# Kernel optimization log

Measured on AMD Instinct MI355X. Metric: run time of the kernel, lower is better.

## Reference

```python
import jax, jax.numpy as jnp
import numpy as np

N = 100_000   # nodes
E = 1_280_000 # edges
F_IN = 64
HID = 64

def setup_inputs() -> dict:
    key = jax.random.key(0)
    ks = jax.random.split(key, 5)
    x = jax.random.normal(ks[0], (N, F_IN), dtype=jnp.float32)
    edge_index = jax.random.randint(ks[1], (2, E), 0, N, dtype=jnp.int32)
    edge_weight = jax.random.uniform(ks[2], (E,), dtype=jnp.float32)
    s1 = 1.0 / np.sqrt(F_IN)
    W1 = jax.random.uniform(ks[3], (F_IN, HID), minval=-s1, maxval=s1, dtype=jnp.float32)
    b1 = jnp.zeros((HID,), jnp.float32)
    s2 = 1.0 / np.sqrt(HID)
    W2 = jax.random.uniform(ks[4], (HID, 1), minval=-s2, maxval=s2, dtype=jnp.float32)
    b2 = jnp.zeros((1,), jnp.float32)
    return {"x": x, "edge_index": edge_index, "edge_weight": edge_weight,
            "W1": W1, "b1": b1, "W2": W2, "b2": b2}


def reference(x, edge_index, edge_weight, W1, b1, W2, b2):
    # eval mode: edge dropout and feature dropout are identity.
    # GCNConv with add_self_loops=True: A_hat = A + I, D_hat^-1/2 A_hat D_hat^-1/2.
    row, col = edge_index[0], edge_index[1]
    sl = jnp.arange(N, dtype=row.dtype)
    row = jnp.concatenate([row, sl])
    col = jnp.concatenate([col, sl])
    w = jnp.concatenate([edge_weight, jnp.ones((N,), edge_weight.dtype)])
    # symmetric normalization (shared by both conv layers)
    deg = jax.ops.segment_sum(w, col, num_segments=N)          # [N]
    dinv = jnp.where(deg > 0, jax.lax.rsqrt(deg), 0.0)
    norm = dinv[row] * w * dinv[col]                           # [E+N]

    def gcn(h):  # h: [N, d] already linearly transformed
        msg = h[row] * norm[:, None]                           # gather + scale
        return jax.ops.segment_sum(msg, col, num_segments=N)   # scatter-add

    h = gcn(x @ W1) + b1          # conv1
    h = jax.nn.relu(h)            # relu (dropout = identity in eval)
    out = gcn(h @ W2) + b2        # conv2 -> [N, 1]
    return out
```

## Files before the change

### kernel.cpp

```cpp
#include <hip/hip_runtime.h>
#include <hip/hip_fp16.h>

#define CNT_SHIFT 26
#define DEG_MASK  ((1u << CNT_SHIFT) - 1)
#define DEG_SCALE 1048576.0f
#define SLAB_LOG 7
#define SLAB 128
#define CAP 2048
#define GSTRIDE 16

typedef __attribute__((ext_vector_type(8))) short short8;
typedef __attribute__((ext_vector_type(4))) float v4f;

__device__ __forceinline__ unsigned short f_to_h16(float f) {
    return __half_as_ushort(__float2half(f));
}
__device__ __forceinline__ float h16_to_f(unsigned short u) {
    return __half2float(__ushort_as_half(u));
}
__device__ __forceinline__ unsigned short f_to_bf16(float f) {
    unsigned int u = __float_as_uint(f);
    u += 0x7fffu + ((u >> 16) & 1u);
    return (unsigned short)(u >> 16);
}
__device__ __forceinline__ unsigned long long mkrec(int r, int c, float wv) {
    return (unsigned long long)r | ((unsigned long long)(c & (SLAB - 1)) << 17)
         | ((unsigned long long)f_to_h16(wv) << 24);
}

__global__ __launch_bounds__(256) void k_scatter_gemm(
        const int4* __restrict__ row4, const int4* __restrict__ col4, const float4* __restrict__ w4,
        const int* __restrict__ row, const int* __restrict__ col, const float* __restrict__ w,
        unsigned* __restrict__ gcur, unsigned long long* __restrict__ binrec,
        const float* __restrict__ x, const float* __restrict__ W1,
        char* __restrict__ h1q, float* __restrict__ scales,
        int E4, int rem, int nBlkE, int nGemm, int n, int nbkt) {
    __shared__ int h[1024];
    int blk = blockIdx.x, t = threadIdx.x;
    if (blk < nBlkE) {
        for (int idx = t; idx < nbkt; idx += 256) h[idx] = 0;
        __syncthreads();
        int base = blk * 1024;
        int4 cs[4];
#pragma unroll
        for (int k = 0; k < 4; ++k) {
            int g = base + k * 256 + t;
            if (g < E4) {
                int4 c = col4[g];
                cs[k] = c;
                atomicAdd(&h[c.x >> SLAB_LOG], 1);
                atomicAdd(&h[c.y >> SLAB_LOG], 1);
                atomicAdd(&h[c.z >> SLAB_LOG], 1);
                atomicAdd(&h[c.w >> SLAB_LOG], 1);
            }
        }
        if (blk == 0 && t < rem) atomicAdd(&h[col[4 * E4 + t] >> SLAB_LOG], 1);
        __syncthreads();
        for (int idx = t; idx < nbkt; idx += 256) {
            int bb = idx + blk;
            while (bb >= nbkt) bb -= nbkt;
            int cnt = h[bb];
            int runbase = 0;
            if (cnt > 0) runbase = (int)atomicAdd(&gcur[(size_t)bb * GSTRIDE], (unsigned)cnt);
            h[bb] = bb * CAP + runbase;
        }
        __syncthreads();
#pragma unroll
        for (int k = 0; k < 4; ++k) {
            int g = base + k * 256 + t;
            if (g < E4) {
                int4   r = row4[g];
                int4   c = cs[k];
                float4 v = w4[g];
                { int pos = atomicAdd(&h[c.x >> SLAB_LOG], 1); binrec[pos] = mkrec(r.x, c.x, v.x); }
                { int pos = atomicAdd(&h[c.y >> SLAB_LOG], 1); binrec[pos] = mkrec(r.y, c.y, v.y); }
                { int pos = atomicAdd(&h[c.z >> SLAB_LOG], 1); binrec[pos] = mkrec(r.z, c.z, v.z); }
                { int pos = atomicAdd(&h[c.w >> SLAB_LOG], 1); binrec[pos] = mkrec(r.w, c.w, v.w); }
            }
        }
        if (blk == 0 && t < rem) {
            int e = 4 * E4 + t;
            int c = col[e];
            int pos = atomicAdd(&h[c >> SLAB_LOG], 1);
            binrec[pos] = mkrec(row[e], c, w[e]);
        }
    } else {
        int b = blk - nBlkE;
        int lane = t & 63;
        int wave = t >> 6;
        int q   = lane >> 4;
        int n16 = lane & 15;
        short8 bf[8];
#pragma unroll
        for (int ct = 0; ct < 4; ++ct) {
#pragma unroll
            for (int hh = 0; hh < 2; ++hh) {
                short8 v;
#pragma unroll
                for (int j = 0; j < 8; ++j)
                    v[j] = (short)f_to_bf16(W1[(hh * 32 + q * 8 + j) * 64 + ct * 16 + n16]);
                bf[ct * 2 + hh] = v;
            }
        }
        int ntile = (n + 15) >> 4;
        int stride = nGemm * 4;
        for (int tile = b * 4 + wave; tile < ntile; tile += stride) {
            int base = tile << 4;
            short8 a0, a1;
            if (base + 16 <= n) {
                const float* xr = x + (size_t)(base + n16) * 64 + q * 8;
                float4 u0 = *(const float4*)(xr);
                float4 u1 = *(const float4*)(xr + 4);
                float4 u2 = *(const float4*)(xr + 32);
                float4 u3 = *(const float4*)(xr + 36);
                a0[0] = (short)f_to_bf16(u0.x); a0[1] = (short)f_to_bf16(u0.y);
                a0[2] = (short)f_to_bf16(u0.z); a0[3] = (short)f_to_bf16(u0.w);
                a0[4] = (short)f_to_bf16(u1.x); a0[5] = (short)f_to_bf16(u1.y);
                a0[6] = (short)f_to_bf16(u1.z); a0[7] = (short)f_to_bf16(u1.w);
                a1[0] = (short)f_to_bf16(u2.x); a1[1] = (short)f_to_bf16(u2.y);
                a1[2] = (short)f_to_bf16(u2.z); a1[3] = (short)f_to_bf16(u2.w);
                a1[4] = (short)f_to_bf16(u3.x); a1[5] = (short)f_to_bf16(u3.y);
                a1[6] = (short)f_to_bf16(u3.z); a1[7] = (short)f_to_bf16(u3.w);
            } else {
                bool ok = (base + n16) < n;
                const float* xr = x + (size_t)(ok ? (base + n16) : 0) * 64 + q * 8;
#pragma unroll
                for (int j = 0; j < 8; ++j) {
                    a0[j] = ok ? (short)f_to_bf16(xr[j])      : (short)0;
                    a1[j] = ok ? (short)f_to_bf16(xr[32 + j]) : (short)0;
                }
            }
            v4f acc0 = {0.f, 0.f, 0.f, 0.f}, acc1 = acc0, acc2 = acc0, acc3 = acc0;
            acc0 = __builtin_amdgcn_mfma_f32_16x16x32_bf16(a0, bf[0], acc0, 0, 0, 0);
            acc0 = __builtin_amdgcn_mfma_f32_16x16x32_bf16(a1, bf[1], acc0, 0, 0, 0);
            acc1 = __builtin_amdgcn_mfma_f32_16x16x32_bf16(a0, bf[2], acc1, 0, 0, 0);
            acc1 = __builtin_amdgcn_mfma_f32_16x16x32_bf16(a1, bf[3], acc1, 0, 0, 0);
            acc2 = __builtin_amdgcn_mfma_f32_16x16x32_bf16(a0, bf[4], acc2, 0, 0, 0);
            acc2 = __builtin_amdgcn_mfma_f32_16x16x32_bf16(a1, bf[5], acc2, 0, 0, 0);
            acc3 = __builtin_amdgcn_mfma_f32_16x16x32_bf16(a0, bf[6], acc3, 0, 0, 0);
            acc3 = __builtin_amdgcn_mfma_f32_16x16x32_bf16(a1, bf[7], acc3, 0, 0, 0);
#pragma unroll
            for (int r = 0; r < 4; ++r) {
                int rowg = base + q * 4 + r;
                if (rowg >= n) break;
                float m = fmaxf(fmaxf(fabsf(acc0[r]), fabsf(acc1[r])),
                                fmaxf(fabsf(acc2[r]), fabsf(acc3[r])));
                m = fmaxf(m, __shfl_xor(m, 1, 64));
                m = fmaxf(m, __shfl_xor(m, 2, 64));
                m = fmaxf(m, __shfl_xor(m, 4, 64));
                m = fmaxf(m, __shfl_xor(m, 8, 64));
                m = fmaxf(m, 1e-20f);
                float inv = 127.0f / m;
                unsigned char* dst = (unsigned char*)h1q + (size_t)rowg * 64 + n16;
                dst[0]  = (unsigned char)(__float2int_rn(acc0[r] * inv) + 128);
                dst[16] = (unsigned char)(__float2int_rn(acc1[r] * inv) + 128);
                dst[32] = (unsigned char)(__float2int_rn(acc2[r] * inv) + 128);
                dst[48] = (unsigned char)(__float2int_rn(acc3[r] * inv) + 128);
                if (n16 == 0) scales[rowg] = m * (1.0f / 127.0f);
            }
        }
    }
}

__global__ __launch_bounds__(256) void k_bucket(
        const unsigned long long* __restrict__ binrec, const unsigned* __restrict__ gcur,
        float* __restrict__ dinv, int* __restrict__ off, int* __restrict__ bktend,
        unsigned* __restrict__ ep, float* __restrict__ scales,
        int N, int nbkt) {
    __shared__ unsigned cnt[SLAB];
    __shared__ int   loff[SLAB];
    __shared__ int   wtot;
    int b = blockIdx.x, t = threadIdx.x;
    int lane = t & 63;
    int e0 = b * CAP;
    int tot = (int)gcur[(size_t)b * GSTRIDE];
    int e1 = e0 + tot;
    if (t < SLAB) cnt[t] = 0u;
    __syncthreads();
    unsigned epw[8];
    unsigned crk[8];
#pragma unroll
    for (int k = 0; k < 8; ++k) {
        int i = e0 + t + k * 256;
        if (i < e1) {
            unsigned long long rec = binrec[i];
            int cl = (int)((rec >> 17) & (SLAB - 1));
            unsigned hb = (unsigned)((rec >> 24) & 0xFFFF);
            float wv = h16_to_f((unsigned short)hb);
            unsigned old = atomicAdd(&cnt[cl],
                                     (1u << CNT_SHIFT) + (unsigned)(wv * DEG_SCALE + 0.5f));
            unsigned rank = old >> CNT_SHIFT;
            epw[k] = ((unsigned)(rec & 0x1FFFF) << 15) | (hb & 0x7fffu);
            crk[k] = ((unsigned)cl << 16) | rank;
        }
    }
    __syncthreads();
    unsigned pk = 0u;
    int c = 0;
    if (t < SLAB) { pk = cnt[t]; c = (int)(pk >> CNT_SHIFT); }
    int incl = c;
#pragma unroll
    for (int o = 1; o < 64; o <<= 1) {
        int v = __shfl_up(incl, o, 64);
        if (lane >= o) incl += v;
    }
    if (t == 63) wtot = incl;
    __syncthreads();
    if (t >= 64 && t < SLAB) incl += wtot;
    if (t < SLAB) {
        int excl = incl - c;
        loff[t] = excl;
        int id = (b << SLAB_LOG) + t;
        if (id < N) {
            float d = rsqrtf((float)(pk & DEG_MASK) * (1.0f / DEG_SCALE) + 1.0f);
            dinv[id] = d;
            scales[id] *= d;
            off[id] = e0 + excl;
        }
    }
    if (t == 0) bktend[b] = e1;
    __syncthreads();
#pragma unroll
    for (int k = 0; k < 8; ++k) {
        int i = e0 + t + k * 256;
        if (i < e1) {
            int cl   = (int)(crk[k] >> 16);
            int rank = (int)(crk[k] & 0xFFFFu);
            ep[e0 + loff[cl] + rank] = epw[k];
        }
    }
}

__global__ __launch_bounds__(256) void k_agg1(
        const char* __restrict__ h1q_, const float* __restrict__ scales,
        const int* __restrict__ off, const int* __restrict__ bktend,
        const unsigned* __restrict__ ep,
        const float* __restrict__ dinv, const float* __restrict__ b1,
        const float* __restrict__ W2,
        float* __restrict__ h2, int n) {
    const unsigned char* __restrict__ h1q = (const unsigned char*)h1q_;
    __shared__ uint2 tbl[4][4][65];
    int t = threadIdx.x;
    int lane = t & 63, wave = t >> 6, grp = lane >> 4, f15 = lane & 15, fl = f15 * 4;
    int i = blockIdx.x * 16 + wave * 4 + grp;
    bool alive = i < n;
    int s = 0, s1 = 0;
    if (alive) {
        s = off[i];
        s1 = (((i & (SLAB - 1)) == (SLAB - 1)) || (i == n - 1)) ? bktend[i >> SLAB_LOG] : off[i + 1];
    }
    int deg = s1 - s;
    int md = max(deg, __shfl_xor(deg, 16, 64));
    md = max(md, __shfl_xor(md, 32, 64));
    float di = alive ? dinv[i] : 0.f;
    float4 acc = {0.f, 0.f, 0.f, 0.f};
    float S = 0.f;
    if (alive) {
        unsigned q4 = *(const unsigned*)(h1q + ((size_t)i << 6) + fl);
        float si = scales[i];
        acc.x = (float)(q4 & 0xffu)         * si;
        acc.y = (float)((q4 >> 8) & 0xffu)  * si;
        acc.z = (float)((q4 >> 16) & 0xffu) * si;
        acc.w = (float)(q4 >> 24)           * si;
        S = si;
    }
    for (int c0 = 0; c0 < md; c0 += 64) {
        int remg = deg - c0;
        int mrem = md - c0; if (mrem > 64) mrem = 64;
        for (int k = 0; k * 16 < mrem; ++k) {
            int slot = k * 16 + f15;
            unsigned src = 0u; float m = 0.f;
            if (slot < remg) {
                unsigned e = ep[s + c0 + slot];
                src = e >> 15;
                m = scales[src] * h16_to_f((unsigned short)(e & 0x7fffu));
            }
            tbl[wave][grp][slot] = make_uint2(src, __float_as_uint(m));
        }
        for (int j = 0; j < mrem; j += 4) {
            uint2 t0 = tbl[wave][grp][j];
            uint2 t1 = tbl[wave][grp][j + 1];
            uint2 t2 = tbl[wave][grp][j + 2];
            uint2 t3 = tbl[wave][grp][j + 3];
            unsigned q0 = *(const unsigned*)(h1q + ((size_t)t0.x << 6) + fl);
            unsigned q1 = *(const unsigned*)(h1q + ((size_t)t1.x << 6) + fl);
            unsigned q2 = *(const unsigned*)(h1q + ((size_t)t2.x << 6) + fl);
            unsigned q3 = *(const unsigned*)(h1q + ((size_t)t3.x << 6) + fl);
            float m0 = __uint_as_float(t0.y), m1 = __uint_as_float(t1.y);
            float m2 = __uint_as_float(t2.y), m3 = __uint_as_float(t3.y);
            acc.x = fmaf((float)(q0 & 0xffu),         m0, acc.x);
            acc.y = fmaf((float)((q0 >> 8) & 0xffu),  m0, acc.y);
            acc.z = fmaf((float)((q0 >> 16) & 0xffu), m0, acc.z);
            acc.w = fmaf((float)(q0 >> 24),           m0, acc.w);
            acc.x = fmaf((float)(q1 & 0xffu),         m1, acc.x);
            acc.y = fmaf((float)((q1 >> 8) & 0xffu),  m1, acc.y);
            acc.z = fmaf((float)((q1 >> 16) & 0xffu), m1, acc.z);
            acc.w = fmaf((float)(q1 >> 24),           m1, acc.w);
            acc.x = fmaf((float)(q2 & 0xffu),         m2, acc.x);
            acc.y = fmaf((float)((q2 >> 8) & 0xffu),  m2, acc.y);
            acc.z = fmaf((float)((q2 >> 16) & 0xffu), m2, acc.z);
            acc.w = fmaf((float)(q2 >> 24),           m2, acc.w);
            acc.x = fmaf((float)(q3 & 0xffu),         m3, acc.x);
            acc.y = fmaf((float)((q3 >> 8) & 0xffu),  m3, acc.y);
            acc.z = fmaf((float)((q3 >> 16) & 0xffu), m3, acc.z);
            acc.w = fmaf((float)(q3 >> 24),           m3, acc.w);
            S += (m0 + m1) + (m2 + m3);
        }
    }
    acc.x = fmaf(S, -128.f, acc.x);
    acc.y = fmaf(S, -128.f, acc.y);
    acc.z = fmaf(S, -128.f, acc.z);
    acc.w = fmaf(S, -128.f, acc.w);
    float4 bb = *(const float4*)(b1 + fl);
    float4 ww = *(const float4*)(W2 + fl);
    float p = fmaxf(fmaf(di, acc.x, bb.x), 0.f) * ww.x
            + fmaxf(fmaf(di, acc.y, bb.y), 0.f) * ww.y
            + fmaxf(fmaf(di, acc.z, bb.z), 0.f) * ww.z
            + fmaxf(fmaf(di, acc.w, bb.w), 0.f) * ww.w;
#pragma unroll
    for (int o = 1; o < 16; o <<= 1) p += __shfl_xor(p, o, 64);
    if (f15 == 0 && alive) h2[i] = di * p;
}

__global__ void k_agg2(const float* __restrict__ h2,
                       const int* __restrict__ off, const int* __restrict__ bktend,
                       const unsigned* __restrict__ ep, const float* __restrict__ dinv,
                       const float* __restrict__ b2, float* __restrict__ out, int n) {
    int i = blockIdx.x * 256 + threadIdx.x;
    if (i >= n) return;
    float acc = h2[i];
    int s = off[i];
    int s1 = (((i & (SLAB - 1)) == (SLAB - 1)) || (i == n - 1)) ? bktend[i >> SLAB_LOG] : off[i + 1];
    for (; s + 8 <= s1; s += 8) {
        unsigned e0 = ep[s],     e1 = ep[s + 1], e2 = ep[s + 2], e3 = ep[s + 3];
        unsigned e4 = ep[s + 4], e5 = ep[s + 5], e6 = ep[s + 6], e7 = ep[s + 7];
        float v0 = h2[e0 >> 15], v1 = h2[e1 >> 15], v2 = h2[e2 >> 15], v3 = h2[e3 >> 15];
        float v4 = h2[e4 >> 15], v5 = h2[e5 >> 15], v6 = h2[e6 >> 15], v7 = h2[e7 >> 15];
        acc = fmaf(v0, h16_to_f((unsigned short)(e0 & 0x7fff)), acc);
        acc = fmaf(v1, h16_to_f((unsigned short)(e1 & 0x7fff)), acc);
        acc = fmaf(v2, h16_to_f((unsigned short)(e2 & 0x7fff)), acc);
        acc = fmaf(v3, h16_to_f((unsigned short)(e3 & 0x7fff)), acc);
        acc = fmaf(v4, h16_to_f((unsigned short)(e4 & 0x7fff)), acc);
        acc = fmaf(v5, h16_to_f((unsigned short)(e5 & 0x7fff)), acc);
        acc = fmaf(v6, h16_to_f((unsigned short)(e6 & 0x7fff)), acc);
        acc = fmaf(v7, h16_to_f((unsigned short)(e7 & 0x7fff)), acc);
    }
    for (; s + 4 <= s1; s += 4) {
        unsigned e0 = ep[s], e1 = ep[s + 1], e2 = ep[s + 2], e3 = ep[s + 3];
        float v0 = h2[e0 >> 15], v1 = h2[e1 >> 15], v2 = h2[e2 >> 15], v3 = h2[e3 >> 15];
        acc = fmaf(v0, h16_to_f((unsigned short)(e0 & 0x7fff)), acc);
        acc = fmaf(v1, h16_to_f((unsigned short)(e1 & 0x7fff)), acc);
        acc = fmaf(v2, h16_to_f((unsigned short)(e2 & 0x7fff)), acc);
        acc = fmaf(v3, h16_to_f((unsigned short)(e3 & 0x7fff)), acc);
    }
    for (; s < s1; ++s) {
        unsigned e = ep[s];
        acc = fmaf(h2[e >> 15], h16_to_f((unsigned short)(e & 0x7fff)), acc);
    }
    out[i] = dinv[i] * acc + b2[0];
}

extern "C" void kernel_launch(void* const* d_in, const int* in_sizes, int n_in,
                              void* d_out, int out_size, void* d_ws, size_t ws_size,
                              hipStream_t stream) {
    const float* x  = (const float*)d_in[0];
    const int*   ei = (const int*)d_in[1];
    const float* w  = (const float*)d_in[2];
    const float* W1 = (const float*)d_in[3];
    const float* b1 = (const float*)d_in[4];
    const float* W2 = (const float*)d_in[5];
    const float* b2 = (const float*)d_in[6];
    float* out = (float*)d_out;

    const int N = in_sizes[0] / 64;
    const int E = in_sizes[2];
    const int* row = ei;
    const int* col = ei + E;

    const int nbkt  = (N + SLAB - 1) >> SLAB_LOG;
    const int E4    = E / 4;
    const int rem   = E - 4 * E4;
    const int nBlkE = (E4 + 1023) / 1024;
    const int nGemm = 1024;

    char* p = (char*)d_ws;
    auto take = [&](size_t bytes) { char* q = p; p += (bytes + 15) & ~(size_t)15; return q; };
    unsigned long long* binrec = (unsigned long long*)take((size_t)nbkt * CAP * 8);
    unsigned* gcur = (unsigned*)take((size_t)nbkt * GSTRIDE * 4);
    int* bktend  = (int*)take((size_t)nbkt * 4);
    char* h1q    = (char*)take((size_t)N * 64);
    float* scales= (float*)take((size_t)N * 4);
    float* dinv  = (float*)take((size_t)N * 4);
    int*   off   = (int*)take((size_t)(N + 1) * 4);
    unsigned* ep = (unsigned*)take((size_t)nbkt * CAP * 4);
    float* h2    = (float*)take((size_t)N * 4);

    (void)hipMemsetAsync(gcur, 0, (size_t)nbkt * GSTRIDE * 4, stream);
    k_scatter_gemm<<<nBlkE + nGemm, 256, 0, stream>>>(
        (const int4*)row, (const int4*)col, (const float4*)w,
        row, col, w, gcur, binrec, x, W1, h1q, scales,
        E4, rem, nBlkE, nGemm, N, nbkt);
    k_bucket<<<nbkt, 256, 0, stream>>>(binrec, gcur, dinv, off, bktend, ep, scales, N, nbkt);
    k_agg1<<<(N + 15) / 16, 256, 0, stream>>>(h1q, scales, off, bktend, ep, dinv, b1, W2, h2, N);
    k_agg2<<<(N + 255) / 256, 256, 0, stream>>>(h2, off, bktend, ep, dinv, b2, out, N);
}
```

Before: 161.9 us.

## Replace two-level bucket sort with global atomic count, scan, and place

Replaces the slab-binned intermediate records and the per-bucket local sort with three steps. Per-node degree and count come from global atomics, a per-slab scan builds offsets and cursors, and a placement pass scatters packed edge words using atomic cursors. This removes the 8-byte binrec staging buffer and its extra read/write pass. In exchange it relies on heavily contended global atomics per edge, reads the edge arrays twice, and adds a kernel launch. Edge order within a node becomes nondeterministic.

Measured after the change: 270.2 us. 1.67x slower.

```diff
diff --git a/kernel.cpp b/kernel.cpp
--- a/kernel.cpp
+++ b/kernel.cpp
@@ -7,7 +7,6 @@
 #define SLAB_LOG 7
 #define SLAB 128
 #define CAP 2048
-#define GSTRIDE 16
 
 typedef __attribute__((ext_vector_type(8))) short short8;
 typedef __attribute__((ext_vector_type(4))) float v4f;
@@ -23,69 +22,41 @@
     u += 0x7fffu + ((u >> 16) & 1u);
     return (unsigned short)(u >> 16);
 }
-__device__ __forceinline__ unsigned long long mkrec(int r, int c, float wv) {
-    return (unsigned long long)r | ((unsigned long long)(c & (SLAB - 1)) << 17)
-         | ((unsigned long long)f_to_h16(wv) << 24);
-}
-
-__global__ __launch_bounds__(256) void k_scatter_gemm(
-        const int4* __restrict__ row4, const int4* __restrict__ col4, const float4* __restrict__ w4,
-        const int* __restrict__ row, const int* __restrict__ col, const float* __restrict__ w,
-        unsigned* __restrict__ gcur, unsigned long long* __restrict__ binrec,
+__device__ __forceinline__ unsigned packcnt(float wv) {
+    return (1u << CNT_SHIFT) + (unsigned)(wv * DEG_SCALE + 0.5f);
+}
+__device__ __forceinline__ unsigned mkep(int r, float wv) {
+    return ((unsigned)r << 15) | (f_to_h16(wv) & 0x7fffu);
+}
+
+__global__ __launch_bounds__(256) void k_count_gemm(
+        const int4* __restrict__ col4, const float4* __restrict__ w4,
+        const int* __restrict__ col, const float* __restrict__ w,
+        unsigned* __restrict__ cnt,
         const float* __restrict__ x, const float* __restrict__ W1,
         char* __restrict__ h1q, float* __restrict__ scales,
-        int E4, int rem, int nBlkE, int nGemm, int n, int nbkt) {
-    __shared__ int h[1024];
+        int E4, int rem, int nCnt, int nGemm, int n) {
     int blk = blockIdx.x, t = threadIdx.x;
-    if (blk < nBlkE) {
-        for (int idx = t; idx < nbkt; idx += 256) h[idx] = 0;
-        __syncthreads();
+    if (blk < nCnt) {
         int base = blk * 1024;
-        int4 cs[4];
 #pragma unroll
         for (int k = 0; k < 4; ++k) {
             int g = base + k * 256 + t;
             if (g < E4) {
-                int4 c = col4[g];
-                cs[k] = c;
-                atomicAdd(&h[c.x >> SLAB_LOG], 1);
-                atomicAdd(&h[c.y >> SLAB_LOG], 1);
-                atomicAdd(&h[c.z >> SLAB_LOG], 1);
-                atomicAdd(&h[c.w >> SLAB_LOG], 1);
-            }
-        }
-        if (blk == 0 && t < rem) atomicAdd(&h[col[4 * E4 + t] >> SLAB_LOG], 1);
-        __syncthreads();
-        for (int idx = t; idx < nbkt; idx += 256) {
-            int bb = idx + blk;
-            while (bb >= nbkt) bb -= nbkt;
-            int cnt = h[bb];
-            int runbase = 0;
-            if (cnt > 0) runbase = (int)atomicAdd(&gcur[(size_t)bb * GSTRIDE], (unsigned)cnt);
-            h[bb] = bb * CAP + runbase;
-        }
-        __syncthreads();
-#pragma unroll
-        for (int k = 0; k < 4; ++k) {
-            int g = base + k * 256 + t;
-            if (g < E4) {
-                int4   r = row4[g];
-                int4   c = cs[k];
+                int4   c = col4[g];
                 float4 v = w4[g];
-                { int pos = atomicAdd(&h[c.x >> SLAB_LOG], 1); binrec[pos] = mkrec(r.x, c.x, v.x); }
-                { int pos = atomicAdd(&h[c.y >> SLAB_LOG], 1); binrec[pos] = mkrec(r.y, c.y, v.y); }
-                { int pos = atomicAdd(&h[c.z >> SLAB_LOG], 1); binrec[pos] = mkrec(r.z, c.z, v.z); }
-                { int pos = atomicAdd(&h[c.w >> SLAB_LOG], 1); binrec[pos] = mkrec(r.w, c.w, v.w); }
+                atomicAdd(&cnt[c.x], packcnt(v.x));
+                atomicAdd(&cnt[c.y], packcnt(v.y));
+                atomicAdd(&cnt[c.z], packcnt(v.z));
+                atomicAdd(&cnt[c.w], packcnt(v.w));
             }
         }
         if (blk == 0 && t < rem) {
             int e = 4 * E4 + t;
-            int c = col[e];
-            int pos = atomicAdd(&h[c >> SLAB_LOG], 1);
-            binrec[pos] = mkrec(row[e], c, w[e]);
+            atomicAdd(&cnt[col[e]], packcnt(w[e]));
         }
     } else {
-        int b = blk - nBlkE;
+        int b = blk - nCnt;
         int lane = t & 63;
         int wave = t >> 6;
         int q   = lane >> 4;
@@ -162,72 +133,59 @@
     }
 }
 
-__global__ __launch_bounds__(256) void k_bucket(
-        const unsigned long long* __restrict__ binrec, const unsigned* __restrict__ gcur,
-        float* __restrict__ dinv, int* __restrict__ off, int* __restrict__ bktend,
-        unsigned* __restrict__ ep, float* __restrict__ scales,
-        int N, int nbkt) {
-    __shared__ unsigned cnt[SLAB];
-    __shared__ int   loff[SLAB];
-    __shared__ int   wtot;
+__global__ __launch_bounds__(128) void k_scan(
+        const unsigned* __restrict__ cnt,
+        float* __restrict__ dinv, int* __restrict__ off, int* __restrict__ cursor,
+        int* __restrict__ bktend, float* __restrict__ scales, int N) {
+    __shared__ int w0tot;
     int b = blockIdx.x, t = threadIdx.x;
     int lane = t & 63;
     int e0 = b * CAP;
-    int tot = (int)gcur[(size_t)b * GSTRIDE];
-    int e1 = e0 + tot;
-    if (t < SLAB) cnt[t] = 0u;
-    __syncthreads();
-    unsigned epw[8];
-    unsigned crk[8];
-#pragma unroll
-    for (int k = 0; k < 8; ++k) {
-        int i = e0 + t + k * 256;
-        if (i < e1) {
-            unsigned long long rec = binrec[i];
-            int cl = (int)((rec >> 17) & (SLAB - 1));
-            unsigned hb = (unsigned)((rec >> 24) & 0xFFFF);
-            float wv = h16_to_f((unsigned short)hb);
-            unsigned old = atomicAdd(&cnt[cl],
-                                     (1u << CNT_SHIFT) + (unsigned)(wv * DEG_SCALE + 0.5f));
-            unsigned rank = old >> CNT_SHIFT;
-            epw[k] = ((unsigned)(rec & 0x1FFFF) << 15) | (hb & 0x7fffu);
-            crk[k] = ((unsigned)cl << 16) | rank;
-        }
-    }
-    __syncthreads();
-    unsigned pk = 0u;
-    int c = 0;
-    if (t < SLAB) { pk = cnt[t]; c = (int)(pk >> CNT_SHIFT); }
+    unsigned pk = cnt[(b << SLAB_LOG) + t];
+    int c = (int)(pk >> CNT_SHIFT);
     int incl = c;
 #pragma unroll
     for (int o = 1; o < 64; o <<= 1) {
         int v = __shfl_up(incl, o, 64);
         if (lane >= o) incl += v;
     }
-    if (t == 63) wtot = incl;
+    if (t == 63) w0tot = incl;
     __syncthreads();
-    if (t >= 64 && t < SLAB) incl += wtot;
-    if (t < SLAB) {
-        int excl = incl - c;
-        loff[t] = excl;
-        int id = (b << SLAB_LOG) + t;
-        if (id < N) {
-            float d = rsqrtf((float)(pk & DEG_MASK) * (1.0f / DEG_SCALE) + 1.0f);
-            dinv[id] = d;
-            scales[id] *= d;
-            off[id] = e0 + excl;
-        }
-    }
-    if (t == 0) bktend[b] = e1;
-    __syncthreads();
-#pragma unroll
-    for (int k = 0; k < 8; ++k) {
-        int i = e0 + t + k * 256;
-        if (i < e1) {
-            int cl   = (int)(crk[k] >> 16);
-            int rank = (int)(crk[k] & 0xFFFFu);
-            ep[e0 + loff[cl] + rank] = epw[k];
-        }
+    if (t >= 64) incl += w0tot;
+    int excl = incl - c;
+    int id = (b << SLAB_LOG) + t;
+    if (id < N) {
+        float d = rsqrtf((float)(pk & DEG_MASK) * (1.0f / DEG_SCALE) + 1.0f);
+        dinv[id] = d;
+        scales[id] *= d;
+        off[id] = e0 + excl;
+        cursor[id] = e0 + excl;
+    }
+    if (t == 127) bktend[b] = e0 + incl;
+}
+
+__global__ __launch_bounds__(256) void k_place(
+        const int4* __restrict__ row4, const int4* __restrict__ col4, const float4* __restrict__ w4,
+        const int* __restrict__ row, const int* __restrict__ col, const float* __restrict__ w,
+        int* __restrict__ cursor, unsigned* __restrict__ ep, int E4, int rem) {
+    int g = blockIdx.x * 256 + threadIdx.x;
+    if (g < E4) {
+        int4   r = row4[g];
+        int4   c = col4[g];
+        float4 v = w4[g];
+        int p0 = atomicAdd(&cursor[c.x], 1);
+        int p1 = atomicAdd(&cursor[c.y], 1);
+        int p2 = atomicAdd(&cursor[c.z], 1);
+        int p3 = atomicAdd(&cursor[c.w], 1);
+        ep[p0] = mkep(r.x, v.x);
+        ep[p1] = mkep(r.y, v.y);
+        ep[p2] = mkep(r.z, v.z);
+        ep[p3] = mkep(r.w, v.w);
+    }
+    if (blockIdx.x == 0 && threadIdx.x < rem) {
+        int e = 4 * E4 + threadIdx.x;
+        int pos = atomicAdd(&cursor[col[e]], 1);
+        ep[pos] = mkep(row[e], w[e]);
     }
 }
 
@@ -380,13 +338,14 @@
     const int nbkt  = (N + SLAB - 1) >> SLAB_LOG;
     const int E4    = E / 4;
     const int rem   = E - 4 * E4;
-    const int nBlkE = (E4 + 1023) / 1024;
+    const int nCnt  = (E4 + 1023) / 1024;
     const int nGemm = 1024;
+    const int nPlace = (E4 + 255) / 256;
 
     char* p = (char*)d_ws;
     auto take = [&](size_t bytes) { char* q = p; p += (bytes + 15) & ~(size_t)15; return q; };
-    unsigned long long* binrec = (unsigned long long*)take((size_t)nbkt * CAP * 8);
-    unsigned* gcur = (unsigned*)take((size_t)nbkt * GSTRIDE * 4);
+    unsigned* cnt  = (unsigned*)take((size_t)nbkt * SLAB * 4);
+    int* cursor  = (int*)take((size_t)nbkt * SLAB * 4);
     int* bktend  = (int*)take((size_t)nbkt * 4);
     char* h1q    = (char*)take((size_t)N * 64);
     float* scales= (float*)take((size_t)N * 4);
@@ -395,12 +354,14 @@
     unsigned* ep = (unsigned*)take((size_t)nbkt * CAP * 4);
     float* h2    = (float*)take((size_t)N * 4);
 
-    (void)hipMemsetAsync(gcur, 0, (size_t)nbkt * GSTRIDE * 4, stream);
-    k_scatter_gemm<<<nBlkE + nGemm, 256, 0, stream>>>(
+    (void)hipMemsetAsync(cnt, 0, (size_t)nbkt * SLAB * 4, stream);
+    k_count_gemm<<<nCnt + nGemm, 256, 0, stream>>>(
+        (const int4*)col, (const float4*)w, col, w, cnt,
+        x, W1, h1q, scales, E4, rem, nCnt, nGemm, N);
+    k_scan<<<nbkt, 128, 0, stream>>>(cnt, dinv, off, cursor, bktend, scales, N);
+    k_place<<<nPlace, 256, 0, stream>>>(
         (const int4*)row, (const int4*)col, (const float4*)w,
-        row, col, w, gcur, binrec, x, W1, h1q, scales,
-        E4, rem, nBlkE, nGemm, N, nbkt);
-    k_bucket<<<nbkt, 256, 0, stream>>>(binrec, gcur, dinv, off, bktend, ep, scales, N, nbkt);
+        row, col, w, cursor, ep, E4, rem);
     k_agg1<<<(N + 15) / 16, 256, 0, stream>>>(h1q, scales, off, bktend, ep, dinv, b1, W2, h2, N);
     k_agg2<<<(N + 255) / 256, 256, 0, stream>>>(h2, off, bktend, ep, dinv, b2, out, N);
 }
```

## Replace global atomic bucket reservation with per-block counts and column scan

Applied to the files above, without the earlier changes.

Splits the fused count-and-scatter kernel into three stages: per-block bucket histograms written to a global matrix, a per-bucket prefix scan across blocks, then a scatter kernel that uses the precomputed offsets. This removes the contended global atomicAdd on bucket cursors and the memset, and makes bin placement deterministic. In exchange it adds two kernel launches, an extra pass over col, and a histogram matrix write and read.

Result: faster. 157.4 us (-2.8%).

```diff
diff --git a/kernel.cpp b/kernel.cpp
--- a/kernel.cpp
+++ b/kernel.cpp
@@ -28,10 +28,9 @@
          | ((unsigned long long)f_to_h16(wv) << 24);
 }
 
-__global__ __launch_bounds__(256) void k_scatter_gemm(
-        const int4* __restrict__ row4, const int4* __restrict__ col4, const float4* __restrict__ w4,
-        const int* __restrict__ row, const int* __restrict__ col, const float* __restrict__ w,
-        unsigned* __restrict__ gcur, unsigned long long* __restrict__ binrec,
+__global__ __launch_bounds__(256) void k_count_gemm(
+        const int4* __restrict__ col4, const int* __restrict__ col,
+        int* __restrict__ gcnt,
         const float* __restrict__ x, const float* __restrict__ W1,
         char* __restrict__ h1q, float* __restrict__ scales,
         int E4, int rem, int nBlkE, int nGemm, int n, int nbkt) {
@@ -41,13 +40,11 @@
         for (int idx = t; idx < nbkt; idx += 256) h[idx] = 0;
         __syncthreads();
         int base = blk * 1024;
-        int4 cs[4];
 #pragma unroll
         for (int k = 0; k < 4; ++k) {
             int g = base + k * 256 + t;
             if (g < E4) {
                 int4 c = col4[g];
-                cs[k] = c;
                 atomicAdd(&h[c.x >> SLAB_LOG], 1);
                 atomicAdd(&h[c.y >> SLAB_LOG], 1);
                 atomicAdd(&h[c.z >> SLAB_LOG], 1);
@@ -56,34 +53,8 @@
         }
         if (blk == 0 && t < rem) atomicAdd(&h[col[4 * E4 + t] >> SLAB_LOG], 1);
         __syncthreads();
-        for (int idx = t; idx < nbkt; idx += 256) {
-            int bb = idx + blk;
-            while (bb >= nbkt) bb -= nbkt;
-            int cnt = h[bb];
-            int runbase = 0;
-            if (cnt > 0) runbase = (int)atomicAdd(&gcur[(size_t)bb * GSTRIDE], (unsigned)cnt);
-            h[bb] = bb * CAP + runbase;
-        }
-        __syncthreads();
-#pragma unroll
-        for (int k = 0; k < 4; ++k) {
-            int g = base + k * 256 + t;
-            if (g < E4) {
-                int4   r = row4[g];
-                int4   c = cs[k];
-                float4 v = w4[g];
-                { int pos = atomicAdd(&h[c.x >> SLAB_LOG], 1); binrec[pos] = mkrec(r.x, c.x, v.x); }
-                { int pos = atomicAdd(&h[c.y >> SLAB_LOG], 1); binrec[pos] = mkrec(r.y, c.y, v.y); }
-                { int pos = atomicAdd(&h[c.z >> SLAB_LOG], 1); binrec[pos] = mkrec(r.z, c.z, v.z); }
-                { int pos = atomicAdd(&h[c.w >> SLAB_LOG], 1); binrec[pos] = mkrec(r.w, c.w, v.w); }
-            }
-        }
-        if (blk == 0 && t < rem) {
-            int e = 4 * E4 + t;
-            int c = col[e];
-            int pos = atomicAdd(&h[c >> SLAB_LOG], 1);
-            binrec[pos] = mkrec(row[e], c, w[e]);
-        }
+        for (int idx = t; idx < nbkt; idx += 256)
+            gcnt[(size_t)blk * nbkt + idx] = h[idx];
     } else {
         int b = blk - nBlkE;
         int lane = t & 63;
@@ -159,6 +130,60 @@
                 if (n16 == 0) scales[rowg] = m * (1.0f / 127.0f);
             }
         }
+    }
+}
+
+__global__ __launch_bounds__(256) void k_colscan(
+        int* __restrict__ gcnt, unsigned* __restrict__ gcur, int nBlkE, int nbkt) {
+    int wave = threadIdx.x >> 6, lane = threadIdx.x & 63;
+    int j = blockIdx.x * 4 + wave;
+    if (j >= nbkt) return;
+    int carry = 0;
+    int nr = (nBlkE + 63) / 64;
+    for (int r = 0; r < nr; ++r) {
+        int b = r * 64 + lane;
+        int v = (b < nBlkE) ? gcnt[(size_t)b * nbkt + j] : 0;
+        int incl = v;
+#pragma unroll
+        for (int o = 1; o < 64; o <<= 1) {
+            int u = __shfl_up(incl, o, 64);
+            if (lane >= o) incl += u;
+        }
+        if (b < nBlkE) gcnt[(size_t)b * nbkt + j] = j * CAP + carry + (incl - v);
+        carry += __shfl(incl, 63, 64);
+    }
+    if (lane == 0) gcur[(size_t)j * GSTRIDE] = (unsigned)carry;
+}
+
+__global__ __launch_bounds__(256) void k_scatter(
+        const int4* __restrict__ row4, const int4* __restrict__ col4, const float4* __restrict__ w4,
+        const int* __restrict__ row, const int* __restrict__ col, const float* __restrict__ w,
+        const int* __restrict__ gcnt, unsigned long long* __restrict__ binrec,
+        int E4, int rem, int nbkt) {
+    __shared__ int h[1024];
+    int blk = blockIdx.x, t = threadIdx.x;
+    for (int idx = t; idx < nbkt; idx += 256)
+        h[idx] = gcnt[(size_t)blk * nbkt + idx];
+    __syncthreads();
+    int base = blk * 1024;
+#pragma unroll
+    for (int k = 0; k < 4; ++k) {
+        int g = base + k * 256 + t;
+        if (g < E4) {
+            int4   r = row4[g];
+            int4   c = col4[g];
+            float4 v = w4[g];
+            { int pos = atomicAdd(&h[c.x >> SLAB_LOG], 1); binrec[pos] = mkrec(r.x, c.x, v.x); }
+            { int pos = atomicAdd(&h[c.y >> SLAB_LOG], 1); binrec[pos] = mkrec(r.y, c.y, v.y); }
+            { int pos = atomicAdd(&h[c.z >> SLAB_LOG], 1); binrec[pos] = mkrec(r.z, c.z, v.z); }
+            { int pos = atomicAdd(&h[c.w >> SLAB_LOG], 1); binrec[pos] = mkrec(r.w, c.w, v.w); }
+        }
+    }
+    if (blk == 0 && t < rem) {
+        int e = 4 * E4 + t;
+        int c = col[e];
+        int pos = atomicAdd(&h[c >> SLAB_LOG], 1);
+        binrec[pos] = mkrec(row[e], c, w[e]);
     }
 }
 
@@ -386,6 +411,7 @@
     char* p = (char*)d_ws;
     auto take = [&](size_t bytes) { char* q = p; p += (bytes + 15) & ~(size_t)15; return q; };
     unsigned long long* binrec = (unsigned long long*)take((size_t)nbkt * CAP * 8);
+    int* gcnt    = (int*)take((size_t)nBlkE * nbkt * 4);
     unsigned* gcur = (unsigned*)take((size_t)nbkt * GSTRIDE * 4);
     int* bktend  = (int*)take((size_t)nbkt * 4);
     char* h1q    = (char*)take((size_t)N * 64);
@@ -395,11 +421,13 @@
     unsigned* ep = (unsigned*)take((size_t)nbkt * CAP * 4);
     float* h2    = (float*)take((size_t)N * 4);
 
-    (void)hipMemsetAsync(gcur, 0, (size_t)nbkt * GSTRIDE * 4, stream);
-    k_scatter_gemm<<<nBlkE + nGemm, 256, 0, stream>>>(
+    k_count_gemm<<<nBlkE + nGemm, 256, 0, stream>>>(
+        (const int4*)col, col, gcnt, x, W1, h1q, scales,
+        E4, rem, nBlkE, nGemm, N, nbkt);
+    k_colscan<<<(nbkt + 3) / 4, 256, 0, stream>>>(gcnt, gcur, nBlkE, nbkt);
+    k_scatter<<<nBlkE, 256, 0, stream>>>(
         (const int4*)row, (const int4*)col, (const float4*)w,
-        row, col, w, gcur, binrec, x, W1, h1q, scales,
-        E4, rem, nBlkE, nGemm, N, nbkt);
+        row, col, w, gcnt, binrec, E4, rem, nbkt);
     k_bucket<<<nbkt, 256, 0, stream>>>(binrec, gcur, dinv, off, bktend, ep, scales, N, nbkt);
     k_agg1<<<(N + 15) / 16, 256, 0, stream>>>(h1q, scales, off, bktend, ep, dinv, b1, W2, h2, N);
     k_agg2<<<(N + 255) / 256, 256, 0, stream>>>(h2, off, bktend, ep, dinv, b2, out, N);
```
